# Performance work log

Measured on AMD Instinct MI355X. Metric: run time of the kernel, lower is better.

Reference implementation:

```python
import jax, jax.numpy as jnp
import numpy as np

CLS_NUM = 16
SCALE = 8.0
STRIDE = 5
NO_OBJ_SCALE = 1.0
EPS = 1e-7


def setup_inputs() -> dict:
    key = jax.random.key(0)
    k1, k2, k3, k4, k5, k6, k7, k8 = jax.random.split(key, 8)
    nB, nH, nW = 16, 160, 160
    N = 2048
    predict = jax.random.normal(k1, (nB, 6 + CLS_NUM, nH, nW), dtype=jnp.float32)
    b = jax.random.randint(k2, (N,), 0, nB).astype(jnp.float32)
    c = jax.random.randint(k3, (N,), 0, CLS_NUM).astype(jnp.float32)
    cx = jax.random.uniform(k4, (N,), minval=0.0, maxval=nW * SCALE)
    cy = jax.random.uniform(k5, (N,), minval=0.0, maxval=nH * SCALE)
    w = jax.random.uniform(k6, (N,), minval=8.0, maxval=80.0)
    h = jax.random.uniform(k7, (N,), minval=8.0, maxval=80.0)
    ang = jax.random.uniform(k8, (N,), minval=-np.pi, maxval=np.pi)
    targets = jnp.stack([b, c, cx, cy, w, h, ang], axis=-1).astype(jnp.float32)
    return {"predict": predict, "targets": targets}


def _masks(targets, nB, nH, nW):
    """Vectorized render_map/build_heatmap: per-(class,batch) obj / noobj grid masks."""
    b_idx = targets[:, 0].astype(jnp.int32)
    c_idx = targets[:, 1].astype(jnp.int32)
    cx = targets[:, 2] / SCALE
    cy = targets[:, 3] / SCALE
    w = targets[:, 4] / SCALE
    h = targets[:, 5] / SCALE
    ang = targets[:, 6]
    cos, sin = jnp.cos(ang), jnp.sin(ang)
    xr = cx * cos + cy * sin          # rotated box center
    yr = -cx * sin + cy * cos
    x3, x4 = xr - h / 2, xr + h / 2   # tight bounds
    y3, y4 = yr - w / 2, yr + w / 2
    x1, x2 = x3 - 0.5, x4 + 0.5       # widened bounds (noobj clearing)
    y1, y2 = y3 - 0.5, y4 + 0.5
    gx = jnp.arange(nW, dtype=jnp.float32) + 0.5   # [W]
    gy = jnp.arange(nH, dtype=jnp.float32) + 0.5   # [H]
    # rotated grid coords per box: [N, H, W]
    vx = cos[:, None, None] * gx[None, None, :] + sin[:, None, None] * gy[None, :, None]
    vy = -sin[:, None, None] * gx[None, None, :] + cos[:, None, None] * gy[None, :, None]

    def inside(xl, xh, yl, yh):
        m = (xl[:, None, None] <= vx) & (vx <= xh[:, None, None]) \
            & (yl[:, None, None] <= vy) & (vy <= yh[:, None, None])
        return m.astype(jnp.float32)

    obj_n = inside(x3, x4, y3, y4)    # [N, H, W]
    wide_n = inside(x1, x2, y1, y2)
    seg = c_idx * nB + b_idx
    nseg = CLS_NUM * nB
    obj_sum = jax.ops.segment_sum(obj_n, seg, num_segments=nseg).reshape(CLS_NUM, nB, nH, nW)
    wide_sum = jax.ops.segment_sum(wide_n, seg, num_segments=nseg).reshape(CLS_NUM, nB, nH, nW)
    obj_mask = obj_sum > 0
    noobj_mask = wide_sum == 0
    return obj_mask, noobj_mask


def reference(predict, targets):
    nB, C, nH, nW = predict.shape
    pred = jnp.transpose(predict, (0, 2, 3, 1))  # [B, H, W, C]
    half = (STRIDE - 1) / 2
    x = jax.nn.sigmoid(pred[..., 0]) * STRIDE - half
    y = jax.nn.sigmoid(pred[..., 1]) * STRIDE - half
    w = pred[..., 2]
    h = pred[..., 3]
    p = jax.nn.sigmoid(pred[..., 4]) * 2 - 1
    q = jax.nn.sigmoid(pred[..., 5]) * 2 - 1

    # ---- confidence loss (per class, BCE on obj / noobj cells) ----
    obj_mask, noobj_mask = _masks(targets, nB, nH, nW)     # [Cls, B, H, W]
    conf = jax.nn.sigmoid(jnp.transpose(pred[..., 6:], (3, 0, 1, 2)))  # [Cls, B, H, W]
    confc = jnp.clip(conf, EPS, 1.0 - EPS)
    obj_f = obj_mask.astype(conf.dtype)
    noobj_f = noobj_mask.astype(conf.dtype)
    n_obj = jnp.sum(obj_f, axis=(1, 2, 3))
    n_noobj = jnp.sum(noobj_f, axis=(1, 2, 3))
    loss_obj = jnp.sum(obj_f * (-jnp.log(confc)), axis=(1, 2, 3)) / jnp.maximum(n_obj, 1.0)
    loss_noobj = jnp.sum(noobj_f * (-jnp.log(1.0 - confc)), axis=(1, 2, 3)) / jnp.maximum(n_noobj, 1.0)
    per_cls = jnp.where(n_obj > 0, loss_obj + NO_OBJ_SCALE * loss_noobj, 0.0)
    loss = jnp.sum(per_cls)

    # ---- box decoding (eval output) ----
    score = jax.nn.sigmoid(pred[..., 6:])
    conf_max = jnp.max(score, axis=-1)
    cls_id = jnp.argmax(score, axis=-1).astype(pred.dtype)
    grid_x = jnp.broadcast_to(jnp.arange(nW, dtype=pred.dtype)[None, None, :], (nB, nH, nW))
    grid_y = jnp.broadcast_to(jnp.arange(nH, dtype=pred.dtype)[None, :, None], (nB, nH, nW))
    t = jnp.sqrt((1 + p) / 2 + 1e-16)
    bang = jnp.arctan2(q / (2 * t + 1e-16), t)
    boxes = jnp.stack([
        conf_max,
        cls_id,
        (grid_x + x) * SCALE,
        (grid_y + y) * SCALE,
        jnp.exp(w) * SCALE,
        jnp.exp(h) * SCALE,
        bang,
    ], axis=-1)                      # [B, H, W, 7]
    output = boxes.reshape(nB, nH * nW, 7)
    return (loss, output)
```

## Files before the change

kernel.cpp:

```cpp
#include <hip/hip_runtime.h>
#include <math.h>

#define CLS_NUM 16
#define NB 16
#define NH 160
#define NW 160
#define NCH 22
#define CSZ 25600
#define NT 2048
#define TPB 256
#define NBOXU 1600
#define TILES 40
#define NMASKU 640
#define TCELLS 640
#define CAP 256
#define CLIPV 16.118096f


__device__ __forceinline__ float splus(float x) {
    return fminf(__logf(1.0f + __expf(x)), CLIPV);
}

__global__ __launch_bounds__(TPB) void detect_main(
        const float* __restrict__ predict,
        const float* __restrict__ targets,
        float* __restrict__ out,
        float* __restrict__ streamP,
        float* __restrict__ maskP)
{
    const int tid = threadIdx.x;
    const int bid = blockIdx.x;

    if (bid >= NMASKU) {
        __shared__ float acc_b[16];
        if (tid < 16) acc_b[tid] = 0.f;
        __syncthreads();

        const int ub = bid - NMASKU;
        int b = ub / 100;
        int r = (ub % 100) * TPB + tid;
        const float* pb = predict + (size_t)b * NCH * CSZ + r;
        float p0 = pb[0];
        float p1 = pb[1 * CSZ];
        float p2 = pb[2 * CSZ];
        float p3 = pb[3 * CSZ];
        float p4 = pb[4 * CSZ];
        float p5 = pb[5 * CSZ];
        float raw[16];
        #pragma unroll
        for (int cc = 0; cc < CLS_NUM; cc++) raw[cc] = pb[(6 + cc) * CSZ];

        float bestraw = raw[0]; int bi = 0;
        #pragma unroll
        for (int cc = 1; cc < CLS_NUM; cc++)
            if (raw[cc] > bestraw) { bestraw = raw[cc]; bi = cc; }

        #pragma unroll
        for (int cc = 0; cc < CLS_NUM; cc++) {
            float v = splus(raw[cc]);
            #pragma unroll
            for (int o = 32; o > 0; o >>= 1) v += __shfl_down(v, o);
            if ((tid & 63) == 0) atomicAdd(&acc_b[cc], v);
        }

        float x = 1.0f / (1.0f + __expf(-p0)) * 5.0f - 2.0f;
        float y = 1.0f / (1.0f + __expf(-p1)) * 5.0f - 2.0f;
        float p = 1.0f / (1.0f + __expf(-p4)) * 2.0f - 1.0f;
        float q = 1.0f / (1.0f + __expf(-p5)) * 2.0f - 1.0f;
        float best = 1.0f / (1.0f + __expf(-bestraw));
        float tq = sqrtf((1.0f + p) * 0.5f + 1e-16f);
        float bang = atan2f(q / (2.0f * tq + 1e-16f), tq);
        int i = r / NW, j = r % NW;
        float* o = out + 1 + ((size_t)b * CSZ + r) * 7;
        o[0] = best;
        o[1] = (float)bi;
        o[2] = ((float)j + x) * 8.0f;
        o[3] = ((float)i + y) * 8.0f;
        o[4] = __expf(p2) * 8.0f;
        o[5] = __expf(p3) * 8.0f;
        o[6] = bang;

        __syncthreads();
        if (tid < 16) streamP[ub * 16 + tid] = acc_b[tid];
        return;
    }

    __shared__ float tg[CAP][8];
    __shared__ float acc_s[64];
    __shared__ int cnt_s, pres_s;

    const int u = bid;
    const int b = u / TILES;
    const int band = u - b * TILES;
    const int rb = band * 4;

    if (tid == 0) { cnt_s = 0; pres_s = 0; }
    if (tid < 64) acc_s[tid] = 0.f;
    __syncthreads();

    const float rlo = (float)rb + 0.5f, rhi = (float)rb + 3.5f;
    const float rbc = (float)rb + 2.0f;

    for (int n = tid; n < NT; n += TPB) {
        const float* tp = targets + n * 7;
        if ((int)tp[0] == b) {
            float cy = tp[3] * 0.125f;
            float w  = tp[4] * 0.125f, h = tp[5] * 0.125f;
            float R = 0.5f * sqrtf(w * w + h * h) + 0.75f;
            if (cy + R >= rlo && cy - R <= rhi) {
                float cx = tp[2] * 0.125f;
                float ang = tp[6];
                float cs_ = cosf(ang), sn_ = sinf(ang);
                float xr =  cx * cs_ + cy * sn_;
                float yr = -cx * sn_ + cy * cs_;
                float x3 = xr - h * 0.5f, x4 = xr + h * 0.5f;
                float y3 = yr - w * 0.5f, y4 = yr + w * 0.5f;
                float acs = fabsf(cs_), asn = fabsf(sn_);
                float ex = acs * 79.5f + asn * 1.5f + 1e-3f;
                float ey = acs * 1.5f  + asn * 79.5f + 1e-3f;
                float vxc = cs_ * 80.0f + sn_ * rbc;
                float vyc = cs_ * rbc   - sn_ * 80.0f;
                if (!(vxc + ex < x3 - 0.5f || vxc - ex > x4 + 0.5f ||
                      vyc + ey < y3 - 0.5f || vyc - ey > y4 + 0.5f)) {
                    int slot = atomicAdd(&cnt_s, 1);
                    if (slot < CAP) {
                        tg[slot][0] = cs_; tg[slot][1] = sn_;
                        tg[slot][2] = x3;  tg[slot][3] = x4;
                        tg[slot][4] = y3;  tg[slot][5] = y4;
                        tg[slot][6] = tp[1];
                    }
                }
            }
        }
    }
    __syncthreads();
    const int cnt = min(cnt_s, CAP);

    float gxa[3], gya[3];
    #pragma unroll
    for (int k = 0; k < 3; k++) {
        int cell = tid + k * TPB;
        gxa[k] = (float)(cell % NW) + 0.5f;
        gya[k] = (float)(rb + cell / NW) + 0.5f;
    }
    unsigned m[3] = {0u, 0u, 0u};
    for (int t = 0; t < cnt; t++) {
        float cs_ = tg[t][0], sn_ = tg[t][1];
        float x3 = tg[t][2], x4 = tg[t][3], y3 = tg[t][4], y4 = tg[t][5];
        int cl = (int)tg[t][6];
        #pragma unroll
        for (int k = 0; k < 3; k++) {
            float vx = cs_ * gxa[k] + sn_ * gya[k];
            float vy = cs_ * gya[k] - sn_ * gxa[k];
            float mn = fminf(fminf(vx - x3, x4 - vx), fminf(vy - y3, y4 - vy));
            unsigned add = (mn >= 0.0f ? 1u : 0u) | (mn >= -0.5f ? 0x10000u : 0u);
            m[k] |= add << cl;
        }
    }
    if (tid >= TCELLS - 2 * TPB) m[2] = 0u;

    unsigned any = m[0] | m[1] | m[2];
    #pragma unroll
    for (int o = 32; o > 0; o >>= 1) any |= (unsigned)__shfl_down((int)any, o);
    if ((tid & 63) == 0) atomicOr(&pres_s, (int)any);
    __syncthreads();
    const unsigned pres = (unsigned)pres_s;

    const float* basec = predict + ((size_t)b * NCH + 6) * CSZ + rb * NW;
    for (int c = 0; c < CLS_NUM; c++) {
        if (!(pres & (0x10000u << c))) continue;
        const float* cp = basec + (size_t)c * CSZ;
        float ao = 0.f, no = 0.f, wsub = 0.f, wc = 0.f;
        #pragma unroll
        for (int k = 0; k < 3; k++) {
            int cell = tid + k * TPB;
            bool ob = (m[k] >> c) & 1u;
            bool wb = (m[k] >> (16 + c)) & 1u;
            if ((ob | wb) && cell < TCELLS) {
                float pv = cp[cell];
                if (ob) { ao += splus(-pv);  no += 1.0f; }
                if (wb) { wsub += splus(pv); wc += 1.0f; }
            }
        }
        #pragma unroll
        for (int o = 32; o > 0; o >>= 1) {
            ao   += __shfl_down(ao, o);
            no   += __shfl_down(no, o);
            wsub += __shfl_down(wsub, o);
            wc   += __shfl_down(wc, o);
        }
        if ((tid & 63) == 0) {
            atomicAdd(&acc_s[c * 4 + 0], ao);
            atomicAdd(&acc_s[c * 4 + 1], no);
            atomicAdd(&acc_s[c * 4 + 2], wsub);
            atomicAdd(&acc_s[c * 4 + 3], wc);
        }
    }
    __syncthreads();
    if (tid < 64) maskP[u * 64 + tid] = acc_s[tid];
}

__global__ __launch_bounds__(1024) void finalize_kernel(
        const float* __restrict__ streamP,
        const float* __restrict__ maskP,
        float* __restrict__ out)
{
    __shared__ float st[64][16];
    __shared__ float mt[16][64];
    __shared__ float S16[16];
    __shared__ float M[64];
    const int tid = threadIdx.x;

    float s = 0.f;
    for (int i = tid; i < NBOXU * 16; i += 1024) s += streamP[i];
    st[tid >> 4][tid & 15] = s;

    float sm_ = 0.f;
    for (int i = tid; i < NMASKU * 64; i += 1024) sm_ += maskP[i];
    mt[tid >> 6][tid & 63] = sm_;
    __syncthreads();

    if (tid < 16) {
        float t = 0.f;
        #pragma unroll
        for (int rrr = 0; rrr < 64; rrr++) t += st[rrr][tid];
        S16[tid] = t;
    } else if (tid >= 64 && tid < 128) {
        int v = tid - 64;
        float t = 0.f;
        #pragma unroll
        for (int gg = 0; gg < 16; gg++) t += mt[gg][v];
        M[v] = t;
    }
    __syncthreads();
    if (tid == 0) {
        float L = 0.f;
        for (int c = 0; c < CLS_NUM; c++) {
            float ao   = M[c * 4 + 0];
            float no   = M[c * 4 + 1];
            float wsub = M[c * 4 + 2];
            float wc   = M[c * 4 + 3];
            if (no > 0.f) {
                float nn = 409600.0f - wc;
                L += ao / fmaxf(no, 1.0f) + (S16[c] - wsub) / fmaxf(nn, 1.0f);
            }
        }
        out[0] = L;
    }
}

extern "C" void kernel_launch(void* const* d_in, const int* in_sizes, int n_in,
                              void* d_out, int out_size, void* d_ws, size_t ws_size,
                              hipStream_t stream) {
    const float* predict = (const float*)d_in[0];
    const float* targets = (const float*)d_in[1];
    float* out = (float*)d_out;

    float* streamP = (float*)d_ws;
    float* maskP   = streamP + NBOXU * 16;

    detect_main<<<NBOXU + NMASKU, TPB, 0, stream>>>(predict, targets, out,
                                                    streamP, maskP);
    finalize_kernel<<<1, 1024, 0, stream>>>(streamP, maskP, out);
}
```

Before: 51.87 us.

## Process two pixel groups per box block, reorder block types, use sigmoid-clamp log

Box-decoding blocks now each handle 512 cells, two per thread, with per-class partial sums kept in registers. This halves the number of box blocks and the shuffle reductions and shared-memory atomics per cell. The launch order is swapped so box blocks come first and mask blocks follow. The softplus form is replaced by sigmoid, clamp and log, which matches the reference's epsilon clipping but adds operations per element and register pressure.

```diff
diff --git a/kernel.cpp b/kernel.cpp
--- a/kernel.cpp
+++ b/kernel.cpp
@@ -9,17 +9,13 @@
 #define CSZ 25600
 #define NT 2048
 #define TPB 256
-#define NBOXU 1600
+#define NBOXB 800
 #define TILES 40
 #define NMASKU 640
 #define TCELLS 640
 #define CAP 256
-#define CLIPV 16.118096f
-
-
-__device__ __forceinline__ float splus(float x) {
-    return fminf(__logf(1.0f + __expf(x)), CLIPV);
-}
+#define EPS_F 1e-7f
+
 
 __global__ __launch_bounds__(TPB) void detect_main(
         const float* __restrict__ predict,
@@ -31,57 +27,70 @@
     const int tid = threadIdx.x;
     const int bid = blockIdx.x;
 
-    if (bid >= NMASKU) {
+    if (bid < NBOXB) {
         __shared__ float acc_b[16];
         if (tid < 16) acc_b[tid] = 0.f;
         __syncthreads();
 
-        const int ub = bid - NMASKU;
-        int b = ub / 100;
-        int r = (ub % 100) * TPB + tid;
-        const float* pb = predict + (size_t)b * NCH * CSZ + r;
-        float p0 = pb[0];
-        float p1 = pb[1 * CSZ];
-        float p2 = pb[2 * CSZ];
-        float p3 = pb[3 * CSZ];
-        float p4 = pb[4 * CSZ];
-        float p5 = pb[5 * CSZ];
-        float raw[16];
-        #pragma unroll
-        for (int cc = 0; cc < CLS_NUM; cc++) raw[cc] = pb[(6 + cc) * CSZ];
-
-        float bestraw = raw[0]; int bi = 0;
-        #pragma unroll
-        for (int cc = 1; cc < CLS_NUM; cc++)
-            if (raw[cc] > bestraw) { bestraw = raw[cc]; bi = cc; }
+        const int b = bid / 50;
+        const int rbase = (bid % 50) * 512;
+        float anS[16];
+        #pragma unroll
+        for (int cc = 0; cc < CLS_NUM; cc++) anS[cc] = 0.f;
+
+        #pragma unroll
+        for (int k = 0; k < 2; k++) {
+            const int r = rbase + k * 256 + tid;
+            const float* pb = predict + (size_t)b * NCH * CSZ + r;
+            float p0 = pb[0];
+            float p1 = pb[1 * CSZ];
+            float p2 = pb[2 * CSZ];
+            float p3 = pb[3 * CSZ];
+            float p4 = pb[4 * CSZ];
+            float p5 = pb[5 * CSZ];
+            float raw[16];
+            #pragma unroll
+            for (int cc = 0; cc < CLS_NUM; cc++) raw[cc] = pb[(6 + cc) * CSZ];
+
+            float bestraw = raw[0]; int bi = 0;
+            #pragma unroll
+            for (int cc = 1; cc < CLS_NUM; cc++)
+                if (raw[cc] > bestraw) { bestraw = raw[cc]; bi = cc; }
+
+            #pragma unroll
+            for (int cc = 0; cc < CLS_NUM; cc++) {
+                float s  = 1.0f / (1.0f + __expf(-raw[cc]));
+                float sc = fminf(fmaxf(s, EPS_F), 1.0f - EPS_F);
+                anS[cc] += -__logf(1.0f - sc);
+            }
+
+            float x = 1.0f / (1.0f + __expf(-p0)) * 5.0f - 2.0f;
+            float y = 1.0f / (1.0f + __expf(-p1)) * 5.0f - 2.0f;
+            float p = 1.0f / (1.0f + __expf(-p4)) * 2.0f - 1.0f;
+            float q = 1.0f / (1.0f + __expf(-p5)) * 2.0f - 1.0f;
+            float best = 1.0f / (1.0f + __expf(-bestraw));
+            float tq = sqrtf((1.0f + p) * 0.5f + 1e-16f);
+            float bang = atan2f(q / (2.0f * tq + 1e-16f), tq);
+            int i = r / NW, j = r % NW;
+            float* o = out + 1 + ((size_t)b * CSZ + r) * 7;
+            o[0] = best;
+            o[1] = (float)bi;
+            o[2] = ((float)j + x) * 8.0f;
+            o[3] = ((float)i + y) * 8.0f;
+            o[4] = __expf(p2) * 8.0f;
+            o[5] = __expf(p3) * 8.0f;
+            o[6] = bang;
+        }
 
         #pragma unroll
         for (int cc = 0; cc < CLS_NUM; cc++) {
-            float v = splus(raw[cc]);
+            float v = anS[cc];
             #pragma unroll
             for (int o = 32; o > 0; o >>= 1) v += __shfl_down(v, o);
             if ((tid & 63) == 0) atomicAdd(&acc_b[cc], v);
         }
-
-        float x = 1.0f / (1.0f + __expf(-p0)) * 5.0f - 2.0f;
-        float y = 1.0f / (1.0f + __expf(-p1)) * 5.0f - 2.0f;
-        float p = 1.0f / (1.0f + __expf(-p4)) * 2.0f - 1.0f;
-        float q = 1.0f / (1.0f + __expf(-p5)) * 2.0f - 1.0f;
-        float best = 1.0f / (1.0f + __expf(-bestraw));
-        float tq = sqrtf((1.0f + p) * 0.5f + 1e-16f);
-        float bang = atan2f(q / (2.0f * tq + 1e-16f), tq);
-        int i = r / NW, j = r % NW;
-        float* o = out + 1 + ((size_t)b * CSZ + r) * 7;
-        o[0] = best;
-        o[1] = (float)bi;
-        o[2] = ((float)j + x) * 8.0f;
-        o[3] = ((float)i + y) * 8.0f;
-        o[4] = __expf(p2) * 8.0f;
-        o[5] = __expf(p3) * 8.0f;
-        o[6] = bang;
-
         __syncthreads();
-        if (tid < 16) streamP[ub * 16 + tid] = acc_b[tid];
+        if (tid < 16) streamP[bid * 16 + tid] = acc_b[tid];
         return;
     }
 
@@ -89,7 +98,7 @@
     __shared__ float acc_s[64];
     __shared__ int cnt_s, pres_s;
 
-    const int u = bid;
+    const int u = bid - NBOXB;
     const int b = u / TILES;
     const int band = u - b * TILES;
     const int rb = band * 4;
@@ -178,8 +187,10 @@
             bool wb = (m[k] >> (16 + c)) & 1u;
             if ((ob | wb) && cell < TCELLS) {
                 float pv = cp[cell];
-                if (ob) { ao += splus(-pv);  no += 1.0f; }
-                if (wb) { wsub += splus(pv); wc += 1.0f; }
+                float s  = 1.0f / (1.0f + __expf(-pv));
+                float sc = fminf(fmaxf(s, EPS_F), 1.0f - EPS_F);
+                if (ob) { ao -= __logf(sc);          no += 1.0f; }
+                if (wb) { wsub -= __logf(1.0f - sc); wc += 1.0f; }
             }
         }
         #pragma unroll
@@ -212,7 +223,7 @@
     const int tid = threadIdx.x;
 
     float s = 0.f;
-    for (int i = tid; i < NBOXU * 16; i += 1024) s += streamP[i];
+    for (int i = tid; i < NBOXB * 16; i += 1024) s += streamP[i];
     st[tid >> 4][tid & 15] = s;
 
     float sm_ = 0.f;
@@ -257,9 +268,9 @@
     float* out = (float*)d_out;
 
     float* streamP = (float*)d_ws;
-    float* maskP   = streamP + NBOXU * 16;
-
-    detect_main<<<NBOXU + NMASKU, TPB, 0, stream>>>(predict, targets, out,
+    float* maskP   = streamP + NBOXB * 16;
+
+    detect_main<<<NBOXB + NMASKU, TPB, 0, stream>>>(predict, targets, out,
                                                     streamP, maskP);
     finalize_kernel<<<1, 1024, 0, stream>>>(streamP, maskP, out);
 }
```

After: 55.04 us. +6.1%, slower.
